# Optimization experiments

Measured on AMD Instinct MI355X. Metric: run time of the kernel, lower is better.

Reference implementation:

```python
import math
import jax, jax.numpy as jnp
import numpy as np

FACTOR = 2  # init kwarg `factor`

def setup_inputs() -> dict:
    key = jax.random.key(0)
    k1, k2, k3 = jax.random.split(key, 3)
    B, H, L, E = 32, 8, 2048, 64
    Q = jax.random.normal(k1, (B, H, L, E), dtype=jnp.float32)
    K = jax.random.normal(k2, (B, H, L, E), dtype=jnp.float32)
    V = jax.random.normal(k3, (B, H, L, E), dtype=jnp.float32)
    return {"Q": Q, "K": K, "V": V}

def _autocorrelation(Q, K, V):
    # Q, K, V: [B, H, L, E]; S == L so the pad/truncate branch is a no-op.
    B, H, L, E = Q.shape
    # FFT-based cross-correlation along the time axis (dim=2)
    q_fft = jnp.fft.rfft(Q, axis=2)
    k_fft = jnp.fft.rfft(K, axis=2)
    corr = jnp.fft.irfft(q_fft * jnp.conj(k_fft), n=L, axis=2)  # [B,H,L,E]
    # time_delay_agg
    top_k = int(FACTOR * math.log(L))  # = 15 for L=2048
    # torch.topk over dim=2 per (b,h,e): move L to last axis for lax.top_k
    weights, delays = jax.lax.top_k(jnp.swapaxes(corr, 2, 3), top_k)  # [B,H,E,k]
    weights = jax.nn.softmax(weights, axis=-1)
    # V.repeat(1,1,2,1) + gather(init+delay) is equivalent to a circular
    # gather from V with index (l + delay) mod L, since 0 <= init+delay <= 2L-2.
    base = jnp.arange(L)  # [L]
    out = jnp.zeros_like(V)
    for i in range(top_k):  # small fixed loop over top_k delays
        d_i = delays[..., i]                       # [B,H,E]
        idx = (base[None, None, :, None] + d_i[:, :, None, :]) % L  # [B,H,L,E]
        pattern = jnp.take_along_axis(V, idx, axis=2)               # [B,H,L,E]
        out = out + pattern * weights[..., i][:, :, None, :]
    return out

def reference(Q, K, V):
    return _autocorrelation(Q, K, V)
```

## Files before the change

### kernel.cpp

```cpp
#include <hip/hip_runtime.h>
#include <math.h>


#define LEN   2048
#define BH    256
#define NE    64
#define NSER  (BH * NE)
#define TOPK  15
#define NINF  (-INFINITY)

__device__ __forceinline__ int PC(int c) { return c + (c >> 4); }

__device__ __forceinline__ void sincos_tw(int idx, float& c, float& s) {
  float ang = (float)idx * (-6.283185307179586f / 2048.0f);
  __sincosf(ang, &s, &c);
}

template <bool INV>
__device__ __forceinline__ void dft8(float* xr, float* xi) {
  const float sg = INV ? -1.f : 1.f;
  const float c = 0.70710678118654752440f;
  float s0r = xr[0] + xr[4], s0i = xi[0] + xi[4];
  float s1r = xr[0] - xr[4], s1i = xi[0] - xi[4];
  float s2r = xr[2] + xr[6], s2i = xi[2] + xi[6];
  float s3r = xr[2] - xr[6], s3i = xi[2] - xi[6];
  float E0r = s0r + s2r, E0i = s0i + s2i;
  float E2r = s0r - s2r, E2i = s0i - s2i;
  float E1r = s1r + sg * s3i, E1i = s1i - sg * s3r;
  float E3r = s1r - sg * s3i, E3i = s1i + sg * s3r;
  float u0r = xr[1] + xr[5], u0i = xi[1] + xi[5];
  float u1r = xr[1] - xr[5], u1i = xi[1] - xi[5];
  float u2r = xr[3] + xr[7], u2i = xi[3] + xi[7];
  float u3r = xr[3] - xr[7], u3i = xi[3] - xi[7];
  float O0r = u0r + u2r, O0i = u0i + u2i;
  float O2r = u0r - u2r, O2i = u0i - u2i;
  float O1r = u1r + sg * u3i, O1i = u1i - sg * u3r;
  float O3r = u1r - sg * u3i, O3i = u1i + sg * u3r;
  float G0r = O0r, G0i = O0i;
  float G1r = O1r * c + O1i * (sg * c), G1i = O1i * c - O1r * (sg * c);
  float G2r = sg * O2i, G2i = -sg * O2r;
  float G3r = -O3r * c + O3i * (sg * c), G3i = -O3i * c - O3r * (sg * c);
  xr[0] = E0r + G0r; xi[0] = E0i + G0i;
  xr[1] = E1r + G1r; xi[1] = E1i + G1i;
  xr[2] = E2r + G2r; xi[2] = E2i + G2i;
  xr[3] = E3r + G3r; xi[3] = E3i + G3i;
  xr[4] = E0r - G0r; xi[4] = E0i - G0i;
  xr[5] = E1r - G1r; xi[5] = E1i - G1i;
  xr[6] = E2r - G2r; xi[6] = E2i - G2i;
  xr[7] = E3r - G3r; xi[7] = E3i - G3i;
}

template <bool INV>
__device__ __forceinline__ void dft4(float* xr, float* xi) {
  const float sg = INV ? -1.f : 1.f;
  float s0r = xr[0] + xr[2], s0i = xi[0] + xi[2];
  float s1r = xr[0] - xr[2], s1i = xi[0] - xi[2];
  float s2r = xr[1] + xr[3], s2i = xi[1] + xi[3];
  float s3r = xr[1] - xr[3], s3i = xi[1] - xi[3];
  xr[0] = s0r + s2r;        xi[0] = s0i + s2i;
  xr[1] = s1r + sg * s3i;   xi[1] = s1i - sg * s3r;
  xr[2] = s0r - s2r;        xi[2] = s0i - s2i;
  xr[3] = s1r - sg * s3i;   xi[3] = s1i + sg * s3r;
}

template <bool INV>
__device__ __forceinline__ void stage8_ip(float2* CB, int s, int sLog, int t) {
  float ar[8], ai[8];
#pragma unroll
  for (int r = 0; r < 8; ++r) {
    float2 v = CB[PC(t + 256 * r)];
    ar[r] = v.x; ai[r] = v.y;
  }
  __syncthreads();
  dft8<INV>(ar, ai);
  int q = t & (s - 1), p = t >> sLog;
  int ob = q + 8 * s * p;
  float c1, s1; sincos_tw(s * p, c1, s1);
  if (INV) s1 = -s1;
  CB[PC(ob)] = make_float2(ar[0], ai[0]);
  float wc = c1, wsn = s1;
#pragma unroll
  for (int j = 1; j < 8; ++j) {
    float zr = ar[j] * wc - ai[j] * wsn;
    float zi = ar[j] * wsn + ai[j] * wc;
    CB[PC(ob + s * j)] = make_float2(zr, zi);
    if (j < 7) {
      float nc = wc * c1 - wsn * s1;
      wsn = wc * s1 + wsn * c1;
      wc = nc;
    }
  }
  __syncthreads();
}


__global__ __launch_bounds__(256) void ktrans_qk(const float* __restrict__ Q,
                                                 const float* __restrict__ K,
                                                 float2* __restrict__ ZT) {
  int bh = blockIdx.x >> 5, l0 = (blockIdx.x & 31) * 64;
  __shared__ float sq[64][65], sk[64][65];
  int t = threadIdx.x;
  const float4* Qb = (const float4*)(Q + ((size_t)bh * LEN + l0) * NE);
  const float4* Kb = (const float4*)(K + ((size_t)bh * LEN + l0) * NE);
  int x = t & 15, c4 = x * 4;
#pragma unroll
  for (int it = 0; it < 4; ++it) {
    int row = (t >> 4) + it * 16;
    float4 q4 = Qb[row * 16 + x];
    float4 k4 = Kb[row * 16 + x];
    sq[row][c4 + 0] = q4.x; sq[row][c4 + 1] = q4.y;
    sq[row][c4 + 2] = q4.z; sq[row][c4 + 3] = q4.w;
    sk[row][c4 + 0] = k4.x; sk[row][c4 + 1] = k4.y;
    sk[row][c4 + 2] = k4.z; sk[row][c4 + 3] = k4.w;
  }
  __syncthreads();
  float2* Zb = ZT + (size_t)bh * NE * LEN + l0;
  int l2 = (t & 31) * 2;
#pragma unroll
  for (int it = 0; it < 8; ++it) {
    int e = (t >> 5) + it * 8;
    float4 o;
    o.x = sq[l2][e];     o.y = sk[l2][e];
    o.z = sq[l2 + 1][e]; o.w = sk[l2 + 1][e];
    *(float4*)&Zb[(size_t)e * LEN + l2] = o;
  }
}

__global__ __launch_bounds__(256) void ktrans_v(const float* __restrict__ src,
                                                float* __restrict__ dst) {
  int bh = blockIdx.x >> 5, l0 = (blockIdx.x & 31) * 64;
  __shared__ float sT[64][65];
  int t = threadIdx.x;
  const float4* Sb = (const float4*)(src + ((size_t)bh * LEN + l0) * NE);
  int x = t & 15, c4 = x * 4;
#pragma unroll
  for (int it = 0; it < 4; ++it) {
    int row = (t >> 4) + it * 16;
    float4 v4 = Sb[row * 16 + x];
    sT[row][c4 + 0] = v4.x; sT[row][c4 + 1] = v4.y;
    sT[row][c4 + 2] = v4.z; sT[row][c4 + 3] = v4.w;
  }
  __syncthreads();
  float* Db = dst + (size_t)bh * NE * LEN + l0;
  int l4 = x * 4;
#pragma unroll
  for (int it = 0; it < 4; ++it) {
    int e = (t >> 4) + it * 16;
    float4 o;
    o.x = sT[l4 + 0][e]; o.y = sT[l4 + 1][e];
    o.z = sT[l4 + 2][e]; o.w = sT[l4 + 3][e];
    *(float4*)&Db[(size_t)e * LEN + l4] = o;
  }
}


__global__ __launch_bounds__(256, 6) void kfft(const float2* __restrict__ ZT,
                                               float* __restrict__ Wt,
                                               int* __restrict__ Dl) {
  __shared__ float2 CB[2176];
  __shared__ float mv[64]; __shared__ int mi[64];
  const int t = threadIdx.x;
  const int wv = t >> 6, ln = t & 63;
  const float2* z = ZT + (size_t)blockIdx.x * LEN;

  {
    float ar[8], ai[8];
#pragma unroll
    for (int r = 0; r < 8; ++r) {
      float2 v = z[t + 256 * r];
      ar[r] = v.x; ai[r] = v.y;
    }
    dft8<false>(ar, ai);
    float c1, s1; sincos_tw(t, c1, s1);
    CB[PC(8 * t)] = make_float2(ar[0], ai[0]);
    float wc = c1, wsn = s1;
#pragma unroll
    for (int j = 1; j < 8; ++j) {
      float zr = ar[j] * wc - ai[j] * wsn;
      float zi = ar[j] * wsn + ai[j] * wc;
      CB[PC(8 * t + j)] = make_float2(zr, zi);
      if (j < 7) {
        float nc = wc * c1 - wsn * s1;
        wsn = wc * s1 + wsn * c1;
        wc = nc;
      }
    }
  }
  __syncthreads();
  stage8_ip<false>(CB, 8, 3, t);
  stage8_ip<false>(CB, 64, 6, t);
#pragma unroll
  for (int h = 0; h < 2; ++h) {
    int u = t + 256 * h;
    float xr[4], xi[4];
#pragma unroll
    for (int r = 0; r < 4; ++r) {
      float2 v = CB[PC(u + 512 * r)];
      xr[r] = v.x; xi[r] = v.y;
    }
    dft4<false>(xr, xi);
#pragma unroll
    for (int j = 0; j < 4; ++j) CB[PC(u + 512 * j)] = make_float2(xr[j], xi[j]);
  }
  __syncthreads();

  {
    float2 zf[4], zm[4];
#pragma unroll
    for (int r = 0; r < 4; ++r) {
      int f = t + 256 * r;
      int m = (LEN - f) & (LEN - 1);
      zf[r] = CB[PC(f)]; zm[r] = CB[PC(m)];
    }
    float2 e1 = make_float2(0.f, 0.f);
    if (t == 0) e1 = CB[PC(1024)];
    __syncthreads();
#pragma unroll
    for (int r = 0; r < 4; ++r) {
      int f = t + 256 * r;
      int m = (LEN - f) & (LEN - 1);
      float Xr = 0.5f * (zf[r].x + zm[r].x), Xi = 0.5f * (zf[r].y - zm[r].y);
      float Yr = 0.5f * (zf[r].y + zm[r].y), Yi = -0.5f * (zf[r].x - zm[r].x);
      CB[PC(f)] = make_float2(Xr * Yr + Xi * Yi, Xi * Yr - Xr * Yi);
      float Xr2 = 0.5f * (zm[r].x + zf[r].x), Xi2 = 0.5f * (zm[r].y - zf[r].y);
      float Yr2 = 0.5f * (zf[r].y + zm[r].y), Yi2 = -0.5f * (zm[r].x - zf[r].x);
      CB[PC(m)] = make_float2(Xr2 * Yr2 + Xi2 * Yi2, Xi2 * Yr2 - Xr2 * Yi2);
    }
    if (t == 0) CB[PC(1024)] = make_float2(e1.x * e1.y, 0.f);
  }
  __syncthreads();

  stage8_ip<true>(CB, 1, 0, t);
  stage8_ip<true>(CB, 8, 3, t);
  stage8_ip<true>(CB, 64, 6, t);
  float rv[8]; int ri[8];
#pragma unroll
  for (int h = 0; h < 2; ++h) {
    int u = t + 256 * h;
    float xr[4], xi[4];
#pragma unroll
    for (int r = 0; r < 4; ++r) {
      float2 v = CB[PC(u + 512 * r)];
      xr[r] = v.x; xi[r] = v.y;
    }
    dft4<true>(xr, xi);
#pragma unroll
    for (int j = 0; j < 4; ++j) {
      rv[h * 4 + j] = xr[j];
      ri[h * 4 + j] = u + 512 * j;
    }
  }

#define CE(i, j) { bool sw = rv[i] < rv[j];                                   \
    float tv = sw ? rv[j] : rv[i]; rv[j] = sw ? rv[i] : rv[j]; rv[i] = tv;    \
    int tx = sw ? ri[j] : ri[i];  ri[j] = sw ? ri[i] : ri[j];  ri[i] = tx; }
  CE(0,1) CE(2,3) CE(4,5) CE(6,7)
  CE(0,2) CE(1,3) CE(4,6) CE(5,7)
  CE(1,2) CE(5,6)
  CE(0,4) CE(1,5) CE(2,6) CE(3,7)
  CE(2,4) CE(3,5)
  CE(1,2) CE(3,4) CE(5,6)
#undef CE

  for (int it = 0; it < TOPK; ++it) {
    float bv = rv[0]; int bidx = ri[0];
#pragma unroll
    for (int off = 32; off >= 1; off >>= 1) {
      float ov = __shfl_xor(bv, off);
      int oi = __shfl_xor(bidx, off);
      bool btr = (ov > bv) || (ov == bv && oi < bidx);
      if (btr) { bv = ov; bidx = oi; }
    }
    if (ln == 0) { mv[wv * 16 + it] = bv; mi[wv * 16 + it] = bidx; }
    if (bidx == ri[0]) {
#pragma unroll
      for (int k = 0; k < 7; ++k) { rv[k] = rv[k + 1]; ri[k] = ri[k + 1]; }
      rv[7] = NINF;
    }
  }
  __syncthreads();

  if (wv == 0) {
    float v = ((ln & 15) < TOPK) ? mv[ln] : NINF;
    int ix = ((ln & 15) < TOPK) ? mi[ln] : 0;
    float myv = NINF; int myi = 0;
    for (int it = 0; it < TOPK; ++it) {
      float bv = v; int bidx = ix;
#pragma unroll
      for (int off = 32; off >= 1; off >>= 1) {
        float ov = __shfl_xor(bv, off);
        int oi = __shfl_xor(bidx, off);
        bool btr = (ov > bv) || (ov == bv && oi < bidx);
        if (btr) { bv = ov; bidx = oi; }
      }
      if (ln == it) { myv = bv; myi = bidx; }
      if (ix == bidx) v = NINF;
    }
    const float scl = 1.0f / 2048.0f;
    float vmax = __shfl(myv, 0);
    float e = (ln < TOPK) ? expf((myv - vmax) * scl) : 0.f;
    float ssum = e;
#pragma unroll
    for (int off = 1; off < 16; off <<= 1) ssum += __shfl_xor(ssum, off);
    if (ln < TOPK) {
      Wt[(size_t)blockIdx.x * 16 + ln] = e / ssum;
      Dl[(size_t)blockIdx.x * 16 + ln] = myi;
    }
  }
}


__global__ __launch_bounds__(256) void kgather_out(const float* __restrict__ VT,
                                                   const float* __restrict__ Wt,
                                                   const int* __restrict__ Dl,
                                                   float* __restrict__ out) {
  const int w = blockIdx.x;
  const int s = (w & 7) * 2048 + (w >> 3);
  const int bh = s >> 6, e = s & 63;
  __shared__ float v[LEN];
  const int t = threadIdx.x;
  const float4* src = (const float4*)(VT + (size_t)s * LEN);
  float4* vv = (float4*)v;
#pragma unroll
  for (int i = 0; i < 2; ++i) vv[t + 256 * i] = src[t + 256 * i];
  float wgt[TOPK]; int d[TOPK];
#pragma unroll
  for (int i = 0; i < TOPK; ++i) {
    wgt[i] = Wt[(size_t)s * 16 + i];
    d[i] = Dl[(size_t)s * 16 + i];
  }
  __syncthreads();
  float* dst = out + ((size_t)bh * LEN) * NE + e;
#pragma unroll
  for (int r = 0; r < 8; ++r) {
    int l = t + 256 * r;
    float acc = 0.f;
#pragma unroll
    for (int i = 0; i < TOPK; ++i) acc += wgt[i] * v[(l + d[i]) & (LEN - 1)];
    dst[(size_t)l * NE] = acc;
  }
}

extern "C" void kernel_launch(void* const* d_in, const int* in_sizes, int n_in,
                              void* d_out, int out_size, void* d_ws, size_t ws_size,
                              hipStream_t stream) {
  const float* Q = (const float*)d_in[0];
  const float* K = (const float*)d_in[1];
  const float* V = (const float*)d_in[2];
  float* out = (float*)d_out;
  char* ws = (char*)d_ws;

  const size_t ZT_BYTES = (size_t)NSER * LEN * sizeof(float2);
  float2* ZT = (float2*)ws;
  float* Wt = (float*)(ws + ZT_BYTES);
  int* Dl = (int*)(ws + ZT_BYTES + (size_t)NSER * 16 * sizeof(float));
  float* VT = (float*)ws;

  ktrans_qk<<<BH * 32, 256, 0, stream>>>(Q, K, ZT);
  kfft<<<NSER, 256, 0, stream>>>(ZT, Wt, Dl);
  ktrans_v<<<BH * 32, 256, 0, stream>>>(V, VT);
  kgather_out<<<NSER, 256, 0, stream>>>(VT, Wt, Dl, out);
}
```

Before: 859.0 us.

## Write gather output contiguously and transpose it back in a separate kernel

The gather kernel now writes each series contiguously into a workspace buffer instead of using a strided scatter with stride NE into the output. A new tiled LDS transpose kernel then converts that buffer to [B,H,L,E], and the output buffer is reused as scratch for the transposed V. The twiddle sincos is switched to the hardware amdgcn sin/cos builtins, which take revolutions, and the occupancy hint on kfft is removed. This trades the uncoalesced scatter for an extra read and write pass over the output.

```diff
diff --git a/kernel.cpp b/kernel.cpp
--- a/kernel.cpp
+++ b/kernel.cpp
@@ -12,8 +12,14 @@
 __device__ __forceinline__ int PC(int c) { return c + (c >> 4); }
 
 __device__ __forceinline__ void sincos_tw(int idx, float& c, float& s) {
+#if __has_builtin(__builtin_amdgcn_sinf) && __has_builtin(__builtin_amdgcn_cosf)
+  float rev = (float)idx * (-1.0f / 2048.0f);
+  s = __builtin_amdgcn_sinf(rev);
+  c = __builtin_amdgcn_cosf(rev);
+#else
   float ang = (float)idx * (-6.283185307179586f / 2048.0f);
   __sincosf(ang, &s, &c);
+#endif
 }
 
 template <bool INV>
@@ -153,10 +159,37 @@
   }
 }
 
-
-__global__ __launch_bounds__(256, 6) void kfft(const float2* __restrict__ ZT,
-                                               float* __restrict__ Wt,
-                                               int* __restrict__ Dl) {
+__global__ __launch_bounds__(256) void ktrans_o(const float* __restrict__ OT,
+                                                float* __restrict__ out) {
+  int bh = blockIdx.x >> 5, l0 = (blockIdx.x & 31) * 64;
+  __shared__ float sT[64][65];
+  int t = threadIdx.x;
+  const float* Sb = OT + (size_t)bh * NE * LEN + l0;
+  int x = t & 15, l4 = x * 4;
+#pragma unroll
+  for (int it = 0; it < 4; ++it) {
+    int e = (t >> 4) + it * 16;
+    float4 v4 = *(const float4*)&Sb[(size_t)e * LEN + l4];
+    sT[e][l4 + 0] = v4.x; sT[e][l4 + 1] = v4.y;
+    sT[e][l4 + 2] = v4.z; sT[e][l4 + 3] = v4.w;
+  }
+  __syncthreads();
+  float* Ob = out + ((size_t)bh * LEN + l0) * NE;
+  int e4 = x * 4;
+#pragma unroll
+  for (int it = 0; it < 4; ++it) {
+    int row = (t >> 4) + it * 16;
+    float4 o;
+    o.x = sT[e4 + 0][row]; o.y = sT[e4 + 1][row];
+    o.z = sT[e4 + 2][row]; o.w = sT[e4 + 3][row];
+    *(float4*)&Ob[row * NE + e4] = o;
+  }
+}
+
+
+__global__ __launch_bounds__(256) void kfft(const float2* __restrict__ ZT,
+                                            float* __restrict__ Wt,
+                                            int* __restrict__ Dl) {
   __shared__ float2 CB[2176];
   __shared__ float mv[64]; __shared__ int mi[64];
   const int t = threadIdx.x;
@@ -310,34 +343,32 @@
 }
 
 
-__global__ __launch_bounds__(256) void kgather_out(const float* __restrict__ VT,
-                                                   const float* __restrict__ Wt,
-                                                   const int* __restrict__ Dl,
-                                                   float* __restrict__ out) {
-  const int w = blockIdx.x;
-  const int s = (w & 7) * 2048 + (w >> 3);
-  const int bh = s >> 6, e = s & 63;
+__global__ __launch_bounds__(256) void kgather(const float* __restrict__ VT,
+                                               const float* __restrict__ Wt,
+                                               const int* __restrict__ Dl,
+                                               float* __restrict__ OT) {
   __shared__ float v[LEN];
   const int t = threadIdx.x;
-  const float4* src = (const float4*)(VT + (size_t)s * LEN);
+  const int series = blockIdx.x;
+  const float4* src = (const float4*)(VT + (size_t)series * LEN);
   float4* vv = (float4*)v;
 #pragma unroll
   for (int i = 0; i < 2; ++i) vv[t + 256 * i] = src[t + 256 * i];
-  float wgt[TOPK]; int d[TOPK];
+  float w[TOPK]; int d[TOPK];
 #pragma unroll
   for (int i = 0; i < TOPK; ++i) {
-    wgt[i] = Wt[(size_t)s * 16 + i];
-    d[i] = Dl[(size_t)s * 16 + i];
-  }
-  __syncthreads();
-  float* dst = out + ((size_t)bh * LEN) * NE + e;
+    w[i] = Wt[(size_t)series * 16 + i];
+    d[i] = Dl[(size_t)series * 16 + i];
+  }
+  __syncthreads();
+  float* dst = OT + (size_t)series * LEN;
 #pragma unroll
   for (int r = 0; r < 8; ++r) {
     int l = t + 256 * r;
     float acc = 0.f;
 #pragma unroll
-    for (int i = 0; i < TOPK; ++i) acc += wgt[i] * v[(l + d[i]) & (LEN - 1)];
-    dst[(size_t)l * NE] = acc;
+    for (int i = 0; i < TOPK; ++i) acc += w[i] * v[(l + d[i]) & (LEN - 1)];
+    dst[l] = acc;
   }
 }
 
@@ -354,10 +385,12 @@
   float2* ZT = (float2*)ws;
   float* Wt = (float*)(ws + ZT_BYTES);
   int* Dl = (int*)(ws + ZT_BYTES + (size_t)NSER * 16 * sizeof(float));
-  float* VT = (float*)ws;
+  float* VT = out;
+  float* OT = (float*)ws;
 
   ktrans_qk<<<BH * 32, 256, 0, stream>>>(Q, K, ZT);
   kfft<<<NSER, 256, 0, stream>>>(ZT, Wt, Dl);
   ktrans_v<<<BH * 32, 256, 0, stream>>>(V, VT);
-  kgather_out<<<NSER, 256, 0, stream>>>(VT, Wt, Dl, out);
-}
+  kgather<<<NSER, 256, 0, stream>>>(VT, Wt, Dl, OT);
+  ktrans_o<<<BH * 32, 256, 0, stream>>>(OT, out);
+}
```

Result: faster. 794.8 us (-7.5%).
